# Kernel optimization log

Hardware: AMD Instinct MI355X
Metric: run time of the kernel (lower is better)

## Reference

```python
import jax, jax.numpy as jnp
import numpy as np
from jax import lax

# hyperparams (match init_kwargs)
DIM = 192      # dim
QK = 192       # qk_dim
HEADS = 8
GS = 128       # group_size
MLP = 384      # mlp_dim
M = 64         # num_tokens
B, H, W = 4, 128, 128


def setup_inputs() -> dict:
    key = jax.random.key(0)
    ks = jax.random.split(key, 12)
    def n(k, sh, sc=0.02):
        return jax.random.normal(k, sh, dtype=jnp.float32) * sc
    return {
        "x": n(ks[0], (B, DIM, H, W), 1.0),
        "ln_g": jnp.ones((DIM,), jnp.float32),
        "ln_b": jnp.zeros((DIM,), jnp.float32),
        "Wq": n(ks[1], (DIM, QK)),
        "Wk": n(ks[2], (DIM, QK)),
        "Wv": n(ks[3], (DIM, DIM)),
        "Wproj": n(ks[4], (DIM, DIM)),
        "Wkg": n(ks[5], (DIM, QK)),      # IRCA global-key projection of means
        "Wvg": n(ks[6], (DIM, DIM)),     # IRCA global-value projection of means
        "means": n(ks[7], (M, DIM), 1.0),  # token dictionary buffer
        "Wconv": n(ks[8], (DIM, DIM)),   # 1x1 conv (no bias) as matrix
        "mlp_ln_g": jnp.ones((DIM,), jnp.float32),
        "mlp_ln_b": jnp.zeros((DIM,), jnp.float32),
        "W_fc1": n(ks[9], (DIM, MLP)),
        "dw": n(ks[10], (MLP, 1, 3, 3)),  # depthwise 3x3 in ConvFFN
        "W_fc2": n(ks[11], (MLP, DIM)),
    }


def _ln(x, g, b, eps=1e-5):
    mu = x.mean(-1, keepdims=True)
    var = ((x - mu) ** 2).mean(-1, keepdims=True)
    return (x - mu) * lax.rsqrt(var + eps) * g + b


def _attn(q, k, v):
    scale = q.shape[-1] ** -0.5
    s = jnp.einsum('...qd,...kd->...qk', q, k) * scale
    p = jax.nn.softmax(s, axis=-1)
    return jnp.einsum('...qk,...kd->...qd', p, v)


def reference(x, ln_g, ln_b, Wq, Wk, Wv, Wproj, Wkg, Wvg, means,
              Wconv, mlp_ln_g, mlp_ln_b, W_fc1, dw, W_fc2):
    b, C, h, w = x.shape
    N = h * w
    xt = x.reshape(b, C, N).transpose(0, 2, 1)          # b n c
    residual = xt
    xn = _ln(xt, ln_g, ln_b)

    # IRCA: per-head global K/V from the token dictionary (means)
    kg = (means @ Wkg).reshape(M, HEADS, QK // HEADS).transpose(1, 0, 2)   # h m dq
    vg = (means @ Wvg).reshape(M, HEADS, C // HEADS).transpose(1, 0, 2)    # h m dv

    # cluster assignment (no-grad): cosine sim to means, argsort by cluster id
    xs = lax.stop_gradient(xn)
    ms = lax.stop_gradient(means)
    xs_n = xs / (jnp.linalg.norm(xs, axis=-1, keepdims=True) + 1e-12)
    ms_n = ms / (jnp.linalg.norm(ms, axis=-1, keepdims=True) + 1e-12)
    belong = jnp.argmax(xs_n @ ms_n.T, axis=-1)          # b n
    idx = jnp.argsort(belong, axis=-1)                   # b n, cluster-sorted order

    # IASA: project, gather into cluster-sorted order
    q = jnp.take_along_axis(xn @ Wq, idx[:, :, None], axis=1)
    k = jnp.take_along_axis(xn @ Wk, idx[:, :, None], axis=1)
    v = jnp.take_along_axis(xn @ Wv, idx[:, :, None], axis=1)

    gs = min(N, GS)
    ng = (N + gs - 1) // gs
    pad_n = ng * gs - N
    pq = jnp.concatenate([q, q[:, N - pad_n:N][:, ::-1]], axis=1)
    pq = pq.reshape(b, ng, gs, HEADS, -1).transpose(0, 1, 3, 2, 4)  # b ng h gs dq

    def windows(t):
        tr = jnp.concatenate([t, t[:, N - pad_n - gs:N][:, ::-1]], axis=1)  # len ng*gs+gs
        t1 = tr[:, :ng * gs].reshape(b, ng, gs, -1)
        t2 = tr[:, gs:].reshape(b, ng, gs, -1)
        tw = jnp.concatenate([t1, t2], axis=2)           # b ng 2gs c
        return tw.reshape(b, ng, 2 * gs, HEADS, -1).transpose(0, 1, 3, 2, 4)

    kw, vw = windows(k), windows(v)
    out1 = _attn(pq, kw, vw)                             # local overlapping windows
    out2 = _attn(pq, kg[None, None], vg[None, None])     # global dictionary attention
    out = (out1 + out2).transpose(0, 1, 3, 2, 4).reshape(b, ng * gs, C)[:, :N]

    # scatter back to original token order (idx is a permutation)
    inv = jnp.argsort(idx, axis=-1)
    out = jnp.take_along_axis(out, inv[:, :, None], axis=1)
    out = (out @ Wproj) @ Wconv                           # proj + 1x1 conv (no bias)
    xt = residual + out

    # PreNorm ConvFFN: LN -> fc1 -> depthwise 3x3 -> GELU -> fc2, residual
    h1 = _ln(xt, mlp_ln_g, mlp_ln_b) @ W_fc1              # b n mlp
    himg = h1.transpose(0, 2, 1).reshape(b, MLP, h, w)
    dwc = lax.conv_general_dilated(himg, dw, (1, 1), 'SAME',
                                   feature_group_count=MLP,
                                   dimension_numbers=('NCHW', 'OIHW', 'NCHW'))
    h2 = jax.nn.gelu(dwc.reshape(b, MLP, N).transpose(0, 2, 1))
    xt = xt + h2 @ W_fc2
    return xt.transpose(0, 2, 1).reshape(b, C, h, w)
```

## Files before the change

kernel.cpp:

```cpp
#include <hip/hip_runtime.h>

using u16 = unsigned short;
using u32 = unsigned int;
typedef __attribute__((ext_vector_type(8))) short short8;
typedef __attribute__((ext_vector_type(4))) short s16x4;
typedef __attribute__((ext_vector_type(4))) float f32x4;
typedef __attribute__((ext_vector_type(2))) float f32x2;
typedef __attribute__((ext_vector_type(4))) u16 u16x4;
typedef __attribute__((ext_vector_type(4))) u32 u32x4;

constexpr int CB   = 4;
constexpr int CC   = 192;
constexpr int CN   = 16384;
constexpr int BN   = CB * CN;
constexpr int CMLP = 384;

__device__ __forceinline__ float b2f(u16 u){ return __uint_as_float(((u32)u) << 16); }
__device__ __forceinline__ u16 f2b(float f){
  u32 u = __float_as_uint(f);
  u32 r = (u + 0x7FFFu + ((u >> 16) & 1u)) >> 16;
  return (u16)r;
}
__device__ __forceinline__ short8 ld8(const u16* p) {
  s16x4 a = *(const s16x4*)p;
  s16x4 b = *(const s16x4*)(p + 4);
  short8 r;
  r[0]=a[0]; r[1]=a[1]; r[2]=a[2]; r[3]=a[3];
  r[4]=b[0]; r[5]=b[1]; r[6]=b[2]; r[7]=b[3];
  return r;
}
__device__ __forceinline__ u32 pk_bf16(float lo, float hi) {
  u32 r;
  asm("v_cvt_pk_bf16_f32 %0, %1, %2" : "=v"(r) : "v"(lo), "v"(hi));
  return r;
}
__device__ __forceinline__ float exp2_fast(float x) {
  float r;
  asm("v_exp_f32 %0, %1" : "=v"(r) : "v"(x));
  return r;
}
__device__ __forceinline__ void gl_lds16(const u16* g, u16* l) {
  __builtin_amdgcn_global_load_lds(
      (const __attribute__((address_space(1))) void*)(const void*)g,
      (__attribute__((address_space(3))) void*)(void*)l, 16, 0, 0);
}

template<int DOARG>
__global__ __launch_bounds__(256) void ln_k(const float* __restrict__ src,
    const float* __restrict__ gg, const float* __restrict__ bb, u16* __restrict__ out,
    const u16* __restrict__ msnT, int* __restrict__ belong)
{
  __shared__ float t[64 * 193];
  __shared__ float sg[192], sb[192];
  __shared__ float smu[64], srs[64];
  const int tid = threadIdx.x;
  const int blk = blockIdx.x;
  const int b = blk >> 8;
  const int n0 = (blk & 255) * 64;
  if (tid < 192) { sg[tid] = gg[tid]; sb[tid] = bb[tid]; }
  const size_t sbase = ((size_t)b * CC) * CN + n0;
  #pragma unroll
  for (int it = 0; it < 48; ++it) {
    int c = it * 4 + (tid >> 6);
    int tok = tid & 63;
    t[tok * 193 + c] = src[sbase + (size_t)c * CN + tok];
  }
  __syncthreads();
  {
    int tok = tid >> 2, sub = tid & 3;
    float s = 0.f, sq = 0.f;
    #pragma unroll
    for (int i = 0; i < 48; ++i) {
      float v = t[tok * 193 + sub * 48 + i];
      s += v; sq += v * v;
    }
    s  += __shfl_xor(s, 1);  s  += __shfl_xor(s, 2);
    sq += __shfl_xor(sq, 1); sq += __shfl_xor(sq, 2);
    float mu = s * (1.f / 192.f);
    float var = fmaxf(sq * (1.f / 192.f) - mu * mu, 0.f);
    float rs = rsqrtf(var + 1e-5f);
    if (sub == 0) { smu[tok] = mu; srs[tok] = rs; }
  }
  __syncthreads();
  const size_t obase = ((size_t)(b * CN + n0)) * CC;
  #pragma unroll
  for (int it = 0; it < 48; ++it) {
    int e = it * 256 + tid;
    int tk = e / 192, c = e % 192;
    float v = (t[tk * 193 + c] - smu[tk]) * srs[tk] * sg[c] + sb[c];
    out[obase + (size_t)tk * CC + c] = f2b(v);
  }

  if (DOARG) {
    const int wv = tid >> 6, lane = tid & 63;
    const int l15 = lane & 15, g4 = lane >> 4, q8 = g4 * 8;
    const int tok = wv * 16 + l15;
    const float mu = smu[tok], rs = srs[tok];
    short8 afm[6];
    #pragma unroll
    for (int ks = 0; ks < 6; ++ks) {
      u32x4 qq;
      #pragma unroll
      for (int j = 0; j < 4; ++j) {
        int c = ks * 32 + q8 + 2 * j;
        float v0 = (t[tok * 193 + c]     - mu) * rs * sg[c]     + sb[c];
        float v1 = (t[tok * 193 + c + 1] - mu) * rs * sg[c + 1] + sb[c + 1];
        qq[j] = pk_bf16(v0, v1);
      }
      afm[ks] = __builtin_bit_cast(short8, qq);
    }
    f32x4 sacc[4];
    #pragma unroll
    for (int ct = 0; ct < 4; ++ct) {
      sacc[ct] = 0.f;
      const u16* pM = msnT + (ct * 16 + l15) * 192 + q8;
      short8 mf[6];
      #pragma unroll
      for (int ks = 0; ks < 6; ++ks) mf[ks] = *(const short8*)(pM + ks * 32);
      #pragma unroll
      for (int ks = 0; ks < 6; ++ks)
        sacc[ct] = __builtin_amdgcn_mfma_f32_16x16x32_bf16(afm[ks], mf[ks], sacc[ct], 0, 0, 0);
    }
    #pragma unroll
    for (int r = 0; r < 4; ++r) {
      float bv = -3e38f; int bi = 1 << 30;
      #pragma unroll
      for (int ct = 0; ct < 4; ++ct) {
        float v = sacc[ct][r];
        int ci = ct * 16 + l15;
        if (v > bv || (v == bv && ci < bi)) { bv = v; bi = ci; }
      }
      #pragma unroll
      for (int d = 1; d < 16; d <<= 1) {
        float ov = __shfl_xor(bv, d);
        int   oi = __shfl_xor(bi, d);
        if (ov > bv || (ov == bv && oi < bi)) { bv = ov; bi = oi; }
      }
      if (l15 == 0) belong[b * CN + n0 + wv * 16 + g4 * 4 + r] = bi;
    }
  }
}

__global__ __launch_bounds__(192) void prep_means_k(const float* __restrict__ means,
    const float* __restrict__ Wkg, const float* __restrict__ Wvg,
    u16* __restrict__ msnT, float* __restrict__ kg, float* __restrict__ vg)
{
  __shared__ float sv[192];
  __shared__ float red[192];
  const int m = blockIdx.x, c = threadIdx.x;
  float v = means[m * 192 + c];
  sv[c] = v; red[c] = v * v;
  __syncthreads();
  for (int s = 96; s >= 3; s >>= 1) {
    if (c < s) red[c] += red[c + s];
    __syncthreads();
  }
  if (c == 0) red[0] = 1.f / (sqrtf(red[0] + red[1] + red[2]) + 1e-12f);
  __syncthreads();
  float scale = red[0];
  msnT[m * 192 + c] = f2b(v * scale);
  float a1 = 0.f, a2 = 0.f;
  for (int cc = 0; cc < 192; ++cc) {
    float mv = sv[cc];
    a1 += mv * Wkg[cc * 192 + c];
    a2 += mv * Wvg[cc * 192 + c];
  }
  int h = c / 24, d = c % 24;
  kg[h * (64 * 24) + m * 24 + d] = a1;
  vg[h * (64 * 24) + m * 24 + d] = a2;
}

__global__ __launch_bounds__(256) void wpcT_k(const float* __restrict__ Wp,
    const float* __restrict__ Wc, u16* __restrict__ WpcT)
{
  int e = blockIdx.x * 256 + threadIdx.x;
  if (e >= 192 * 192) return;
  int i = e / 192, j = e % 192;
  float a = 0.f;
  for (int k = 0; k < 192; ++k) a += Wp[i * 192 + k] * Wc[k * 192 + j];
  WpcT[j * 192 + i] = f2b(a);
}

__global__ __launch_bounds__(256) void wT_k(const float* __restrict__ W,
    u16* __restrict__ dst, int K, int NCsrc, int jcount)
{
  int e = blockIdx.x * 256 + threadIdx.x;
  if (e >= K * jcount) return;
  int j = e / K, k = e % K;
  dst[e] = f2b(W[k * NCsrc + j]);
}

enum { EP_QKV = 0, EP_RESID = 2, EP_H1 = 3, EP_FINAL = 4 };

template<int KTOT, int NCOLS, int EPI>
__global__ __launch_bounds__(256) void gemm3_k(const u16* __restrict__ A,
    const u16* __restrict__ Wt, const float* __restrict__ resid,
    void* __restrict__ outp, int astride)
{
  __shared__ __attribute__((aligned(16))) u16 lA[64 * 192];
  constexpr int KC = KTOT / 192;
  constexpr int WCOLS = NCOLS / 4;
  constexpr int WCT = WCOLS / 16;
  constexpr int NACC = (KC == 2) ? WCT * 4 : 4;
  const int tid = threadIdx.x;
  const int row0 = blockIdx.y * 64;
  const int b = row0 >> 14;
  const int col0 = blockIdx.x * NCOLS;
  const int wv = tid >> 6, lane = tid & 63;
  const int l15 = lane & 15, g4 = lane >> 4, q8 = g4 * 8;
  const int colw = col0 + wv * WCOLS;

  f32x4 acc[NACC];
  #pragma unroll
  for (int i = 0; i < NACC; ++i) acc[i] = 0.f;

  #pragma unroll
  for (int kc = 0; kc < KC; ++kc) {
    if (kc) __syncthreads();
    #pragma unroll
    for (int j = 0; j < 6; ++j) {
      int C = (wv * 6 + j) * 64 + lane;
      int r = C / 24;
      int c = C - r * 24;
      const u16* gp = A + (size_t)(row0 + r) * astride + kc * 192 + c * 8;
      gl_lds16(gp, lA + (wv * 6 + j) * 512);
    }
    __syncthreads();
    short8 af[4][6];
    #pragma unroll
    for (int rt = 0; rt < 4; ++rt)
      #pragma unroll
      for (int ks = 0; ks < 6; ++ks)
        af[rt][ks] = *(const short8*)(lA + (rt * 16 + l15) * 192 + ks * 32 + q8);

    #pragma unroll
    for (int jc = 0; jc < WCT; ++jc) {
      const u16* pW = Wt + (size_t)(colw + jc * 16 + l15) * KTOT + kc * 192 + q8;
      short8 wf[6];
      #pragma unroll
      for (int ks = 0; ks < 6; ++ks) wf[ks] = *(const short8*)(pW + ks * 32);
      #pragma unroll
      for (int ks = 0; ks < 6; ++ks)
        #pragma unroll
        for (int rt = 0; rt < 4; ++rt) {
          int ai = (KC == 2) ? jc * 4 + rt : rt;
          if (EPI == EP_FINAL || EPI == EP_RESID)
            acc[ai] = __builtin_amdgcn_mfma_f32_16x16x32_bf16(wf[ks], af[rt][ks], acc[ai], 0, 0, 0);
          else
            acc[ai] = __builtin_amdgcn_mfma_f32_16x16x32_bf16(af[rt][ks], wf[ks], acc[ai], 0, 0, 0);
        }

      if (KC == 1 && EPI == EP_QKV) {
        u16* o = (u16*)outp;
        int col = colw + jc * 16 + l15;
        #pragma unroll
        for (int rt = 0; rt < 4; ++rt) {
          int row = row0 + rt * 16 + g4 * 4;
          #pragma unroll
          for (int r = 0; r < 4; ++r)
            o[(size_t)(row + r) * 576 + col] = f2b(acc[rt][r]);
          acc[rt] = 0.f;
        }
      } else if (KC == 1 && EPI == EP_H1) {
        u16* o = (u16*)outp;
        int col = colw + jc * 16 + l15;
        #pragma unroll
        for (int rt = 0; rt < 4; ++rt) {
          int row = row0 + rt * 16 + g4 * 4;
          #pragma unroll
          for (int r = 0; r < 4; ++r)
            o[(size_t)(row + r) * CMLP + col] = f2b(acc[rt][r]);
          acc[rt] = 0.f;
        }
      } else if (KC == 1 && EPI == EP_RESID) {
        float* o = (float*)outp;
        #pragma unroll
        for (int rt = 0; rt < 4; ++rt) {
          int n = ((row0 + rt * 16) & 16383) + l15;
          #pragma unroll
          for (int r = 0; r < 4; ++r) {
            int col = colw + jc * 16 + g4 * 4 + r;
            size_t o2 = ((size_t)(b * CC + col)) * CN + n;
            o[o2] = resid[o2] + acc[rt][r];
          }
          acc[rt] = 0.f;
        }
      }
    }
  }

  if (EPI == EP_FINAL) {
    float* o = (float*)outp;
    #pragma unroll
    for (int jc = 0; jc < WCT; ++jc)
      #pragma unroll
      for (int tt = 0; tt < 4; ++tt) {
        int n = ((row0 + tt * 16) & 16383) + l15;
        #pragma unroll
        for (int r = 0; r < 4; ++r) {
          int outcol = colw + jc * 16 + g4 * 4 + r;
          size_t o2 = ((size_t)(b * CC + outcol)) * CN + n;
          o[o2] = resid[o2] + acc[jc * 4 + tt][r];
        }
      }
  }
}

__global__ __launch_bounds__(256) void hist_k(const int* __restrict__ belong, int* __restrict__ histG)
{
  __shared__ int h[64];
  int tid = threadIdx.x, blk = blockIdx.x;
  if (tid < 64) h[tid] = 0;
  __syncthreads();
  int c = belong[blk * 256 + tid];
  atomicAdd(&h[c], 1);
  __syncthreads();
  if (tid < 64) histG[blk * 64 + tid] = h[tid];
}

__global__ __launch_bounds__(64) void scan_k(const int* __restrict__ histG, int* __restrict__ chunkBase)
{
  int b = blockIdx.x, c = threadIdx.x;
  int tot = 0;
  for (int ch = 0; ch < 64; ++ch) tot += histG[(b * 64 + ch) * 64 + c];
  int inc = tot;
  for (int d = 1; d < 64; d <<= 1) {
    int v = __shfl_up(inc, d);
    if (c >= d) inc += v;
  }
  int run = inc - tot;
  for (int ch = 0; ch < 64; ++ch) {
    chunkBase[(b * 64 + ch) * 64 + c] = run;
    run += histG[(b * 64 + ch) * 64 + c];
  }
}

__global__ __launch_bounds__(256) void rank_k(const int* __restrict__ belong,
    const int* __restrict__ chunkBase, int* __restrict__ idx)
{
  __shared__ int WH[4][64];
  int tid = threadIdx.x, blk = blockIdx.x;
  int b = blk >> 6, chl = blk & 63;
  int wv = tid >> 6, lane = tid & 63;
  ((int*)WH)[tid] = 0;
  __syncthreads();
  int nl = chl * 256 + tid;
  int c = belong[blk * 256 + tid];
  int rank = 0;
  for (int m = 0; m < 64; ++m) {
    unsigned long long msk = __ballot(c == m);
    if (c == m) {
      rank = __popcll(msk & ((1ull << lane) - 1ull));
      if (rank == 0) WH[wv][m] = __popcll(msk);
    }
  }
  __syncthreads();
  int off = 0;
  #pragma unroll
  for (int w = 0; w < 3; ++w) if (w < wv) off += WH[w][c];
  int pos = chunkBase[(b * 64 + chl) * 64 + c] + off + rank;
  idx[b * CN + pos] = nl;
}

__global__ __launch_bounds__(256) void attn_k(u16* __restrict__ qkv,
    const float* __restrict__ kg, const float* __restrict__ vg,
    const int* __restrict__ idx)
{
  __shared__ __attribute__((aligned(16))) u16 sK[320 * 28];
  __shared__ __attribute__((aligned(16))) u16 sVT[24 * 340];
  __shared__ int sidx[256];
  const int g = blockIdx.x, h = blockIdx.y, b = blockIdx.z;
  const int tid = threadIdx.x;
  const int wave = tid >> 6, lane = tid & 63;
  const int l15 = lane & 15, g4 = lane >> 4;
  const int q8 = g4 * 8;
  const size_t base = (size_t)b * CN * 576;
  const float QSC = 0.20412414523193154f * 1.4426950408889634f;
  short8 z8 = {0,0,0,0,0,0,0,0};

  {
    int p = g * 128 + tid;
    if (p >= CN) p = 2 * CN - 1 - p;
    sidx[tid] = idx[b * CN + p];
  }
  __syncthreads();

  #pragma unroll
  for (int it = 0; it < 8; ++it) {
    int e4 = (it * 256 + tid) * 4;
    if (e4 < 7680) {
      int r = e4 / 24, c = e4 % 24;
      if (r < 256) {
        int p = sidx[r];
        *(u16x4*)(sK + r * 28 + c) =
          *(const u16x4*)(qkv + base + (size_t)p * 576 + 192 + h * 24 + c);
      } else {
        const float* kp = kg + h * 1536 + (r - 256) * 24 + c;
        u16x4 o;
        o[0] = f2b(kp[0]); o[1] = f2b(kp[1]); o[2] = f2b(kp[2]); o[3] = f2b(kp[3]);
        *(u16x4*)(sK + r * 28 + c) = o;
      }
    }
  }
  #pragma unroll
  for (int it = 0; it < 8; ++it) {
    int e4 = (it * 256 + tid) * 4;
    if (e4 < 7680) {
      int kk = e4 / 24, c = e4 % 24;
      if (kk < 256) {
        int p = sidx[kk];
        u16x4 v = *(const u16x4*)(qkv + base + (size_t)p * 576 + 384 + h * 24 + c);
        sVT[(c + 0) * 340 + kk] = v[0];
        sVT[(c + 1) * 340 + kk] = v[1];
        sVT[(c + 2) * 340 + kk] = v[2];
        sVT[(c + 3) * 340 + kk] = v[3];
      } else {
        const float* vp = vg + h * 1536 + (kk - 256) * 24 + c;
        sVT[(c + 0) * 340 + kk] = f2b(vp[0]);
        sVT[(c + 1) * 340 + kk] = f2b(vp[1]);
        sVT[(c + 2) * 340 + kk] = f2b(vp[2]);
        sVT[(c + 3) * 340 + kk] = f2b(vp[3]);
      }
    }
  }

  short8 qf[2];
  #pragma unroll
  for (int rt = 0; rt < 2; ++rt) {
    int qrow = sidx[wave * 32 + rt * 16 + l15];
    if (g4 < 3) {
      short8 raw = ld8(qkv + base + (size_t)qrow * 576 + h * 24 + q8);
      u32x4 qq;
      #pragma unroll
      for (int j = 0; j < 4; ++j) {
        float lo = b2f((u16)raw[2 * j]) * QSC;
        float hi = b2f((u16)raw[2 * j + 1]) * QSC;
        qq[j] = pk_bf16(lo, hi);
      }
      qf[rt] = __builtin_bit_cast(short8, qq);
    } else {
      qf[rt] = z8;
    }
  }
  __syncthreads();

  float l1[2] = {0.f, 0.f}, l2[2] = {0.f, 0.f};
  f32x4 O1[2][2], O2[2][2];
  #pragma unroll
  for (int rt = 0; rt < 2; ++rt)
    #pragma unroll
    for (int ct2 = 0; ct2 < 2; ++ct2) { O1[rt][ct2] = 0.f; O2[rt][ct2] = 0.f; }

  const int srow = (lane & 48) + ((lane & 48) >> 2);
  const int srcLo = ((lane & 16) << 1) + l15;
  const int srcHi = srcLo + 16;
  const bool hiSel = lane >= 32;
  f32x4 zz = 0.f;

  auto do_tile = [&](int ktile, float* l, f32x4 (*O)[2]) {
    short8 aK[4];
    #pragma unroll
    for (int ct = 0; ct < 4; ++ct)
      aK[ct] = (g4 < 3) ? ld8(sK + (ktile + ct * 16 + l15) * 28 + q8) : z8;
    short8 bV[2][2];
    #pragma unroll
    for (int kc = 0; kc < 2; ++kc)
      #pragma unroll
      for (int ct2 = 0; ct2 < 2; ++ct2) {
        int vrow = ct2 * 16 + l15;
        bV[kc][ct2] = (vrow < 24) ? ld8(sVT + vrow * 340 + ktile + kc * 32 + q8) : z8;
      }
    #pragma unroll
    for (int rt = 0; rt < 2; ++rt) {
      f32x4 p[4];
      #pragma unroll
      for (int ct = 0; ct < 4; ++ct)
        p[ct] = __builtin_amdgcn_mfma_f32_16x16x32_bf16(aK[ct], qf[rt], zz, 0, 0, 0);
      float ps = 0.f;
      #pragma unroll
      for (int ct = 0; ct < 4; ++ct)
        #pragma unroll
        for (int r = 0; r < 4; ++r) {
          float pe = exp2_fast(p[ct][r]);
          p[ct][r] = pe;
          ps += pe;
        }
      ps += __shfl_xor(ps, 16);
      ps += __shfl_xor(ps, 32);
      l[rt] += ps;
      #pragma unroll
      for (int kc = 0; kc < 2; ++kc) {
        u32 wA0 = pk_bf16(p[kc * 2][0], p[kc * 2][1]);
        u32 wA1 = pk_bf16(p[kc * 2][2], p[kc * 2][3]);
        u32 wB0 = pk_bf16(p[kc * 2 + 1][0], p[kc * 2 + 1][1]);
        u32 wB1 = pk_bf16(p[kc * 2 + 1][2], p[kc * 2 + 1][3]);
        u32 a0 = (u32)__shfl((int)wA0, srcLo), a1 = (u32)__shfl((int)wA1, srcLo);
        u32 a2 = (u32)__shfl((int)wA0, srcHi), a3 = (u32)__shfl((int)wA1, srcHi);
        u32 b0 = (u32)__shfl((int)wB0, srcLo), b1 = (u32)__shfl((int)wB1, srcLo);
        u32 b2 = (u32)__shfl((int)wB0, srcHi), b3 = (u32)__shfl((int)wB1, srcHi);
        u32x4 fr;
        fr[0] = hiSel ? b0 : a0; fr[1] = hiSel ? b1 : a1;
        fr[2] = hiSel ? b2 : a2; fr[3] = hiSel ? b3 : a3;
        short8 aP = __builtin_bit_cast(short8, fr);
        #pragma unroll
        for (int ct2 = 0; ct2 < 2; ++ct2)
          O[rt][ct2] = __builtin_amdgcn_mfma_f32_16x16x32_bf16(aP, bV[kc][ct2], O[rt][ct2], 0, 0, 0);
      }
    }
  };

  do_tile(0,   l1, O1);
  do_tile(64,  l1, O1);
  do_tile(128, l1, O1);
  do_tile(192, l1, O1);
  do_tile(256, l2, O2);

  #pragma unroll
  for (int rt = 0; rt < 2; ++rt) {
    float li1 = 1.f / l1[rt];
    float li2 = 1.f / l2[rt];
    #pragma unroll
    for (int r = 0; r < 4; ++r) {
      float i1 = __shfl(li1, srow + r);
      float i2 = __shfl(li2, srow + r);
      int tok = sidx[wave * 32 + rt * 16 + g4 * 4 + r];
      #pragma unroll
      for (int ct2 = 0; ct2 < 2; ++ct2) {
        int d = ct2 * 16 + l15;
        if (d < 24) {
          float v = O1[rt][ct2][r] * i1 + O2[rt][ct2][r] * i2;
          qkv[base + (size_t)tok * 576 + h * 24 + d] = f2b(v);
        }
      }
    }
  }
}

__global__ __launch_bounds__(256) void conv_k(const u16* __restrict__ h1,
    const float* __restrict__ dw, u16* __restrict__ h2g)
{
  __shared__ float t[1156 * 10];
  __shared__ float sdw[72];
  const int tile = blockIdx.x;
  const int jg = blockIdx.y;
  const int bb = blockIdx.z;
  const int y0 = (tile >> 2) * 32, x0 = (tile & 3) * 32;
  const int tid = threadIdx.x;
  if (tid < 72) sdw[tid] = dw[jg * 72 + tid];
  #pragma unroll
  for (int it = 0; it < 5; ++it) {
    int e = it * 256 + tid;
    if (e < 1156) {
      int yy = e / 34 - 1 + y0, xx = e % 34 - 1 + x0;
      float v[8];
      if (yy >= 0 && yy < 128 && xx >= 0 && xx < 128) {
        short8 raw = *(const short8*)(h1 + ((size_t)(bb * CN + yy * 128 + xx)) * CMLP + jg * 8);
        #pragma unroll
        for (int c = 0; c < 8; ++c) v[c] = b2f((u16)raw[c]);
      } else {
        #pragma unroll
        for (int c = 0; c < 8; ++c) v[c] = 0.f;
      }
      #pragma unroll
      for (int c = 0; c < 8; c += 2) {
        f32x2 p; p[0] = v[c]; p[1] = v[c + 1];
        *(f32x2*)(t + e * 10 + c) = p;
      }
    }
  }
  __syncthreads();
  float acc[4][8];
  #pragma unroll
  for (int px = 0; px < 4; ++px)
    #pragma unroll
    for (int c = 0; c < 8; ++c) acc[px][c] = 0.f;
  #pragma unroll
  for (int k = 0; k < 9; ++k) {
    const int dy = k / 3, dx = k % 3;
    float w[8];
    #pragma unroll
    for (int c = 0; c < 8; ++c) w[c] = sdw[c * 9 + k];
    #pragma unroll
    for (int px = 0; px < 4; ++px) {
      int idx2 = px * 256 + tid;
      int oy = idx2 >> 5, ox = idx2 & 31;
      const float* vp = t + ((oy + dy) * 34 + ox + dx) * 10;
      #pragma unroll
      for (int c = 0; c < 8; ++c) acc[px][c] += vp[c] * w[c];
    }
  }
  #pragma unroll
  for (int px = 0; px < 4; ++px) {
    int idx2 = px * 256 + tid;
    int oy = idx2 >> 5, ox = idx2 & 31;
    short8 o;
    #pragma unroll
    for (int c = 0; c < 8; ++c) {
      float a = acc[px][c];
      float u = 1.5957691216057308f * (a + 0.044715f * a * a * a);
      float gel = a / (1.f + __expf(-u));
      o[c] = (short)f2b(gel);
    }
    *(short8*)(h2g + ((size_t)(bb * CN + (y0 + oy) * 128 + x0 + ox)) * CMLP + jg * 8) = o;
  }
}

extern "C" void kernel_launch(void* const* d_in, const int* in_sizes, int n_in,
                              void* d_out, int out_size, void* d_ws, size_t ws_size,
                              hipStream_t stream)
{
  const float* x     = (const float*)d_in[0];
  const float* ln_g  = (const float*)d_in[1];
  const float* ln_b  = (const float*)d_in[2];
  const float* Wq    = (const float*)d_in[3];
  const float* Wk    = (const float*)d_in[4];
  const float* Wv    = (const float*)d_in[5];
  const float* Wproj = (const float*)d_in[6];
  const float* Wkg   = (const float*)d_in[7];
  const float* Wvg   = (const float*)d_in[8];
  const float* means = (const float*)d_in[9];
  const float* Wconv = (const float*)d_in[10];
  const float* mlp_g = (const float*)d_in[11];
  const float* mlp_b = (const float*)d_in[12];
  const float* Wfc1  = (const float*)d_in[13];
  const float* dw    = (const float*)d_in[14];
  const float* Wfc2  = (const float*)d_in[15];
  float* out = (float*)d_out;
  (void)in_sizes; (void)n_in; (void)out_size; (void)ws_size;

  char* ws = (char*)d_ws;
  size_t off = 0;
  auto alloc = [&](size_t sz) { void* p = ws + off; off += (sz + 255) & ~(size_t)255; return p; };
  u16*  xn    = (u16*)alloc((size_t)BN * 192 * 2);
  u16*  qkv   = (u16*)alloc((size_t)BN * 576 * 2);
  float* xt2  = (float*)alloc((size_t)BN * 192 * 4);
  u16*  h2g   = (u16*)alloc((size_t)BN * 384 * 2);
  u16*  msnT  = (u16*)alloc(64 * 192 * 2);
  u16*  WqkvT = (u16*)alloc(576 * 192 * 2);
  u16*  WpcT  = (u16*)alloc(192 * 192 * 2);
  u16*  Wfc1T = (u16*)alloc(384 * 192 * 2);
  u16*  Wfc2T = (u16*)alloc(192 * 384 * 2);
  float* kg   = (float*)alloc(8 * 64 * 24 * 4);
  float* vg   = (float*)alloc(8 * 64 * 24 * 4);
  int*  belong = (int*)alloc(BN * 4);
  int*  idxb   = (int*)alloc(BN * 4);
  int*  histG  = (int*)alloc(256 * 64 * 4);
  int*  chunkBase = (int*)alloc(256 * 64 * 4);
  u16* ln2 = xn;
  u16* h1  = qkv;

  prep_means_k<<<64, 192, 0, stream>>>(means, Wkg, Wvg, msnT, kg, vg);
  wpcT_k<<<144, 256, 0, stream>>>(Wproj, Wconv, WpcT);
  wT_k<<<144, 256, 0, stream>>>(Wq, WqkvT + 0,             192, 192, 192);
  wT_k<<<144, 256, 0, stream>>>(Wk, WqkvT + 192 * 192,     192, 192, 192);
  wT_k<<<144, 256, 0, stream>>>(Wv, WqkvT + 2 * 192 * 192, 192, 192, 192);
  wT_k<<<288, 256, 0, stream>>>(Wfc1, Wfc1T, 192, 384, 384);
  wT_k<<<288, 256, 0, stream>>>(Wfc2, Wfc2T, 384, 192, 192);

  ln_k<1><<<1024, 256, 0, stream>>>(x, ln_g, ln_b, xn, msnT, belong);
  hist_k<<<256, 256, 0, stream>>>(belong, histG);
  scan_k<<<4, 64, 0, stream>>>(histG, chunkBase);
  rank_k<<<256, 256, 0, stream>>>(belong, chunkBase, idxb);
  gemm3_k<192, 576, EP_QKV><<<dim3(1, 1024), 256, 0, stream>>>(xn, WqkvT, nullptr, qkv, 192);
  attn_k<<<dim3(128, 8, 4), 256, 0, stream>>>(qkv, kg, vg, idxb);
  gemm3_k<192, 192, EP_RESID><<<dim3(1, 1024), 256, 0, stream>>>(qkv, WpcT, x, xt2, 576);
  ln_k<0><<<1024, 256, 0, stream>>>(xt2, mlp_g, mlp_b, ln2, nullptr, nullptr);
  gemm3_k<192, 384, EP_H1><<<dim3(1, 1024), 256, 0, stream>>>(ln2, Wfc1T, nullptr, h1, 192);
  conv_k<<<dim3(16, 48, 4), 256, 0, stream>>>(h1, dw, h2g);
  gemm3_k<384, 192, EP_FINAL><<<dim3(1, 1024), 256, 0, stream>>>(h2g, Wfc2T, xt2, out, 384);
}
```

Baseline: 344.4 us.

## Fuse MLP LayerNorm into residual GEMM epilogue and fold softmax sum into MFMA

The residual projection GEMM now keeps its fp32 outputs in shared memory, computes per-token LayerNorm statistics, and writes the normalized bf16 activations directly. This removes the separate ln_k launch and its reread of xt2. In attention, a row of ones is appended to the transposed V tile so the MFMA produces the softmax denominator, replacing the explicit exp sums and cross-lane shuffles. The cost is more LDS in the resid GEMM, which may reduce occupancy, and a softmax sum accumulated from bf16-rounded probabilities.

```diff
diff --git a/kernel.cpp b/kernel.cpp
--- a/kernel.cpp
+++ b/kernel.cpp
@@ -195,9 +195,15 @@
 template<int KTOT, int NCOLS, int EPI>
 __global__ __launch_bounds__(256) void gemm3_k(const u16* __restrict__ A,
     const u16* __restrict__ Wt, const float* __restrict__ resid,
-    void* __restrict__ outp, int astride)
-{
-  __shared__ __attribute__((aligned(16))) u16 lA[64 * 192];
+    void* __restrict__ outp, int astride,
+    const float* __restrict__ g2, const float* __restrict__ b2, u16* __restrict__ ln2out)
+{
+  constexpr bool LNB = (EPI == EP_RESID);
+  constexpr size_t SH_BYTES = LNB ? (size_t)(64 * 197 * 4) : (size_t)(64 * 192 * 2);
+  __shared__ __attribute__((aligned(16))) char shraw[SH_BYTES];
+  __shared__ float smu2[64], srs2[64];
+  u16*   lA    = (u16*)shraw;
+  float* lnbuf = (float*)shraw;
   constexpr int KC = KTOT / 192;
   constexpr int WCOLS = NCOLS / 4;
   constexpr int WCT = WCOLS / 16;
@@ -232,6 +238,7 @@
       #pragma unroll
       for (int ks = 0; ks < 6; ++ks)
         af[rt][ks] = *(const short8*)(lA + (rt * 16 + l15) * 192 + ks * 32 + q8);
+    if (LNB) __syncthreads();
 
     #pragma unroll
     for (int jc = 0; jc < WCT; ++jc) {
@@ -281,7 +288,9 @@
           for (int r = 0; r < 4; ++r) {
             int col = colw + jc * 16 + g4 * 4 + r;
             size_t o2 = ((size_t)(b * CC + col)) * CN + n;
-            o[o2] = resid[o2] + acc[rt][r];
+            float val = resid[o2] + acc[rt][r];
+            o[o2] = val;
+            lnbuf[(rt * 16 + l15) * 197 + col] = val;
           }
           acc[rt] = 0.f;
         }
@@ -289,7 +298,33 @@
     }
   }
 
-  if (EPI == EP_FINAL) {
+  if (EPI == EP_RESID) {
+    __syncthreads();
+    {
+      int tok = tid >> 2, sub = tid & 3;
+      float s = 0.f, sq = 0.f;
+      #pragma unroll
+      for (int i = 0; i < 48; ++i) {
+        float v = lnbuf[tok * 197 + sub * 48 + i];
+        s += v; sq += v * v;
+      }
+      s  += __shfl_xor(s, 1);  s  += __shfl_xor(s, 2);
+      sq += __shfl_xor(sq, 1); sq += __shfl_xor(sq, 2);
+      float mu = s * (1.f / 192.f);
+      float var = fmaxf(sq * (1.f / 192.f) - mu * mu, 0.f);
+      float rs = rsqrtf(var + 1e-5f);
+      if (sub == 0) { smu2[tok] = mu; srs2[tok] = rs; }
+    }
+    __syncthreads();
+    const size_t obase = (size_t)row0 * CC;
+    #pragma unroll
+    for (int it = 0; it < 48; ++it) {
+      int e = it * 256 + tid;
+      int tk = e / 192, c = e % 192;
+      float v = (lnbuf[tk * 197 + c] - smu2[tk]) * srs2[tk] * g2[c] + b2[c];
+      ln2out[obase + (size_t)tk * CC + c] = f2b(v);
+    }
+  } else if (EPI == EP_FINAL) {
     float* o = (float*)outp;
     #pragma unroll
     for (int jc = 0; jc < WCT; ++jc)
@@ -367,7 +402,7 @@
     const int* __restrict__ idx)
 {
   __shared__ __attribute__((aligned(16))) u16 sK[320 * 28];
-  __shared__ __attribute__((aligned(16))) u16 sVT[24 * 340];
+  __shared__ __attribute__((aligned(16))) u16 sVT[25 * 340];
   __shared__ int sidx[256];
   const int g = blockIdx.x, h = blockIdx.y, b = blockIdx.z;
   const int tid = threadIdx.x;
@@ -383,6 +418,7 @@
     if (p >= CN) p = 2 * CN - 1 - p;
     sidx[tid] = idx[b * CN + p];
   }
+  for (int e = tid; e < 340; e += 256) sVT[24 * 340 + e] = 0x3F80;
   __syncthreads();
 
   #pragma unroll
@@ -444,20 +480,18 @@
   }
   __syncthreads();
 
-  float l1[2] = {0.f, 0.f}, l2[2] = {0.f, 0.f};
   f32x4 O1[2][2], O2[2][2];
   #pragma unroll
   for (int rt = 0; rt < 2; ++rt)
     #pragma unroll
     for (int ct2 = 0; ct2 < 2; ++ct2) { O1[rt][ct2] = 0.f; O2[rt][ct2] = 0.f; }
 
-  const int srow = (lane & 48) + ((lane & 48) >> 2);
   const int srcLo = ((lane & 16) << 1) + l15;
   const int srcHi = srcLo + 16;
   const bool hiSel = lane >= 32;
   f32x4 zz = 0.f;
 
-  auto do_tile = [&](int ktile, float* l, f32x4 (*O)[2]) {
+  auto do_tile = [&](int ktile, f32x4 (*O)[2]) {
     short8 aK[4];
     #pragma unroll
     for (int ct = 0; ct < 4; ++ct)
@@ -468,7 +502,7 @@
       #pragma unroll
       for (int ct2 = 0; ct2 < 2; ++ct2) {
         int vrow = ct2 * 16 + l15;
-        bV[kc][ct2] = (vrow < 24) ? ld8(sVT + vrow * 340 + ktile + kc * 32 + q8) : z8;
+        bV[kc][ct2] = (vrow < 25) ? ld8(sVT + vrow * 340 + ktile + kc * 32 + q8) : z8;
       }
     #pragma unroll
     for (int rt = 0; rt < 2; ++rt) {
@@ -476,18 +510,11 @@
       #pragma unroll
       for (int ct = 0; ct < 4; ++ct)
         p[ct] = __builtin_amdgcn_mfma_f32_16x16x32_bf16(aK[ct], qf[rt], zz, 0, 0, 0);
-      float ps = 0.f;
       #pragma unroll
       for (int ct = 0; ct < 4; ++ct)
         #pragma unroll
-        for (int r = 0; r < 4; ++r) {
-          float pe = exp2_fast(p[ct][r]);
-          p[ct][r] = pe;
-          ps += pe;
-        }
-      ps += __shfl_xor(ps, 16);
-      ps += __shfl_xor(ps, 32);
-      l[rt] += ps;
+        for (int r = 0; r < 4; ++r)
+          p[ct][r] = exp2_fast(p[ct][r]);
       #pragma unroll
       for (int kc = 0; kc < 2; ++kc) {
         u32 wA0 = pk_bf16(p[kc * 2][0], p[kc * 2][1]);
@@ -509,20 +536,21 @@
     }
   };
 
-  do_tile(0,   l1, O1);
-  do_tile(64,  l1, O1);
-  do_tile(128, l1, O1);
-  do_tile(192, l1, O1);
-  do_tile(256, l2, O2);
-
+  do_tile(0,   O1);
+  do_tile(64,  O1);
+  do_tile(128, O1);
+  do_tile(192, O1);
+  do_tile(256, O2);
+
+  const int lsrc = (lane & 48) + 8;
   #pragma unroll
   for (int rt = 0; rt < 2; ++rt) {
-    float li1 = 1.f / l1[rt];
-    float li2 = 1.f / l2[rt];
     #pragma unroll
     for (int r = 0; r < 4; ++r) {
-      float i1 = __shfl(li1, srow + r);
-      float i2 = __shfl(li2, srow + r);
+      float s1 = __shfl(O1[rt][1][r], lsrc);
+      float s2 = __shfl(O2[rt][1][r], lsrc);
+      float i1 = 1.f / s1;
+      float i2 = 1.f / s2;
       int tok = sidx[wave * 32 + rt * 16 + g4 * 4 + r];
       #pragma unroll
       for (int ct2 = 0; ct2 < 2; ++ct2) {
@@ -661,11 +689,10 @@
   hist_k<<<256, 256, 0, stream>>>(belong, histG);
   scan_k<<<4, 64, 0, stream>>>(histG, chunkBase);
   rank_k<<<256, 256, 0, stream>>>(belong, chunkBase, idxb);
-  gemm3_k<192, 576, EP_QKV><<<dim3(1, 1024), 256, 0, stream>>>(xn, WqkvT, nullptr, qkv, 192);
+  gemm3_k<192, 576, EP_QKV><<<dim3(1, 1024), 256, 0, stream>>>(xn, WqkvT, nullptr, qkv, 192, nullptr, nullptr, nullptr);
   attn_k<<<dim3(128, 8, 4), 256, 0, stream>>>(qkv, kg, vg, idxb);
-  gemm3_k<192, 192, EP_RESID><<<dim3(1, 1024), 256, 0, stream>>>(qkv, WpcT, x, xt2, 576);
-  ln_k<0><<<1024, 256, 0, stream>>>(xt2, mlp_g, mlp_b, ln2, nullptr, nullptr);
-  gemm3_k<192, 384, EP_H1><<<dim3(1, 1024), 256, 0, stream>>>(ln2, Wfc1T, nullptr, h1, 192);
+  gemm3_k<192, 192, EP_RESID><<<dim3(1, 1024), 256, 0, stream>>>(qkv, WpcT, x, xt2, 576, mlp_g, mlp_b, ln2);
+  gemm3_k<192, 384, EP_H1><<<dim3(1, 1024), 256, 0, stream>>>(ln2, Wfc1T, nullptr, h1, 192, nullptr, nullptr, nullptr);
   conv_k<<<dim3(16, 48, 4), 256, 0, stream>>>(h1, dw, h2g);
-  gemm3_k<384, 192, EP_FINAL><<<dim3(1, 1024), 256, 0, stream>>>(h2g, Wfc2T, xt2, out, 384);
-}
+  gemm3_k<384, 192, EP_FINAL><<<dim3(1, 1024), 256, 0, stream>>>(h2g, Wfc2T, xt2, out, 384, nullptr, nullptr, nullptr);
+}
```

Result: no change. 339.9 us (-1.3%).
